# Kernel optimization log

Measured on AMD Instinct MI355X. Metric: run time of the kernel, lower is better.

Reference implementation:

```python
import jax, jax.numpy as jnp
import numpy as np

IN_DIM, HID, MEM, OUT = 512, 1024, 1024, 512
BATCH = 4096
HIST = 5  # hist_steps hard-coded in MMU.__init__

_LINEARS = [("inpgate", IN_DIM, HID), ("rec_inpgate", OUT, HID), ("mem_inpgate", MEM, HID),
            ("inp", IN_DIM, HID), ("rec_inp", OUT, HID),
            ("readgate", IN_DIM, MEM), ("rec_readgate", OUT, MEM), ("mem_readgate", MEM, MEM),
            ("decoder", HID, MEM),
            ("writegate", IN_DIM, MEM), ("rec_writegate", OUT, MEM), ("mem_writegate", MEM, MEM),
            ("encoder", MEM, HID)]


def setup_inputs() -> dict:
    key = jax.random.key(0)
    ks = iter(jax.random.split(key, 2 * len(_LINEARS) + 4))
    d = {"input": jax.random.normal(next(ks), (IN_DIM, BATCH), jnp.float32)}
    for name, fin, fout in _LINEARS:
        bound = 1.0 / np.sqrt(fin)  # torch nn.Linear default init range
        d["W_" + name] = jax.random.uniform(next(ks), (fout, fin), jnp.float32, -bound, bound)
        d["b_" + name] = jax.random.uniform(next(ks), (fout,), jnp.float32, -bound, bound)
    d["w_hid_out"] = jax.random.uniform(next(ks), (OUT, MEM), jnp.float32)  # torch.rand
    return d


def reference(input, W_inpgate, b_inpgate, W_rec_inpgate, b_rec_inpgate,
              W_mem_inpgate, b_mem_inpgate, W_inp, b_inp, W_rec_inp, b_rec_inp,
              W_readgate, b_readgate, W_rec_readgate, b_rec_readgate,
              W_mem_readgate, b_mem_readgate, W_decoder, b_decoder,
              W_writegate, b_writegate, W_rec_writegate, b_rec_writegate,
              W_mem_writegate, b_mem_writegate, W_encoder, b_encoder, w_hid_out):
    B = input.shape[1]
    lin = lambda x, W, b: x @ W.T + b
    # fresh module: history is zeros except last slot = current input (transposed to [B, in])
    xs = jnp.concatenate([jnp.zeros((HIST - 1, B, IN_DIM), input.dtype), input.T[None]], axis=0)

    def step(carry, x):
        out, mem = carry  # [B, OUT], [B, MEM]
        block_inp = jax.nn.sigmoid(lin(x, W_inp, b_inp) + lin(out, W_rec_inp, b_rec_inp))
        inp_gate = jax.nn.sigmoid(lin(x, W_inpgate, b_inpgate) + lin(mem, W_mem_inpgate, b_mem_inpgate)
                                  + lin(out, W_rec_inpgate, b_rec_inpgate))
        read_gate = jax.nn.sigmoid(lin(x, W_readgate, b_readgate) + lin(mem, W_mem_readgate, b_mem_readgate)
                                   + lin(out, W_rec_readgate, b_rec_readgate))
        decoded_mem = lin(read_gate * mem, W_decoder, b_decoder)
        hidden = decoded_mem + block_inp * inp_gate  # [B, HID] (HID == MEM)
        write_gate = jax.nn.sigmoid(lin(x, W_writegate, b_writegate) + lin(mem, W_mem_writegate, b_mem_writegate)
                                    + lin(out, W_rec_writegate, b_rec_writegate))
        encoded = jnp.tanh(lin(hidden, W_encoder, b_encoder))
        mem = (1.0 - write_gate) * mem + write_gate * encoded
        out = hidden @ w_hid_out.T  # w_hid_out.mm(hidden.T).T
        return (out, mem), None

    init = (jnp.zeros((B, OUT), input.dtype), jnp.zeros((B, MEM), input.dtype))
    (out, _mem), _ = jax.lax.scan(step, init, xs)
    return out
```

## Files before the change

### kernel.cpp

```cpp
#include <hip/hip_runtime.h>
#include <hip/hip_bf16.h>
#include <math.h>

typedef __hip_bfloat16 bf16;
typedef __attribute__((ext_vector_type(8))) short s16x8;
typedef __attribute__((ext_vector_type(4))) float f32x4;

__device__ __forceinline__ float fsig(float x) {
  return __builtin_amdgcn_rcpf(1.0f + __expf(-x));
}
__device__ __forceinline__ float ftanh(float x) { return 2.0f * fsig(2.0f * x) - 1.0f; }
__device__ __forceinline__ float dot4(float4 a, float4 b) {
  return a.x * b.x + a.y * b.y + a.z * b.z + a.w * b.w;
}

__global__ void setup(const float* __restrict__ W_inp, const float* __restrict__ W_ig,
                      const float* __restrict__ W_rg, const float* __restrict__ W_ho,
                      const float* __restrict__ W_dec, const float* __restrict__ input,
                      const float* __restrict__ b_inp, const float* __restrict__ b_rinp,
                      const float* __restrict__ b_ig, const float* __restrict__ b_mig,
                      const float* __restrict__ b_rig, const float* __restrict__ b_wg,
                      const float* __restrict__ b_mwg, const float* __restrict__ b_rwg,
                      const float* __restrict__ b_dec, bf16* __restrict__ Wcat,
                      bf16* __restrict__ WhoB, bf16* __restrict__ Wcat2, bf16* __restrict__ Wdt,
                      bf16* __restrict__ Xb, float* __restrict__ out_s, float* __restrict__ mem_s,
                      float* __restrict__ hidv, float* __restrict__ wgv,
                      float* __restrict__ vout) {
  __shared__ float t[32][33];
  const int id = blockIdx.x, tid = threadIdx.x;
  if (id < 8198) {
    const int i = id * 256 + tid;
    if (i < 524288) {
      Wcat[i] = __float2bfloat16(W_inp[i]);
    } else if (i < 1048576) {
      Wcat[i] = __float2bfloat16(W_ig[i - 524288]);
    } else if (i < 1572864) {
      Wcat[i] = __float2bfloat16(W_rg[i - 1048576]);
    } else if (i < 2097152) {
      const int k = i - 1572864;
      const bf16 vv = __float2bfloat16(W_ho[k]);
      WhoB[k] = vv;
      Wcat2[(size_t)(k >> 10) * 2048 + (k & 1023)] = vv;
    } else if (i < 2098688) {
      const int tt = i - 2097152;
      if (tt < 512) out_s[tt] = 0.0f;
      else mem_s[tt - 512] = 0.0f;
    }
  } else if (id < 10246) {
    const int b = id - 8198;
    const int i0 = (b >> 7) * 32, b0 = (b & 127) * 32;
    const int tx = tid & 31, ty = tid >> 5;
#pragma unroll
    for (int r = ty; r < 32; r += 8) t[r][tx] = input[(size_t)(i0 + r) * 4096 + b0 + tx];
    __syncthreads();
#pragma unroll
    for (int r = ty; r < 32; r += 8)
      Xb[(size_t)(b0 + r) * 512 + i0 + tx] = __float2bfloat16(t[tx][r]);
  } else if (id < 11270) {
    const int b = id - 10246;
    const int j0 = (b >> 5) * 32, k0 = (b & 31) * 32;
    const int tx = tid & 31, ty = tid >> 5;
#pragma unroll
    for (int r = ty; r < 32; r += 8) t[r][tx] = W_dec[(size_t)(j0 + r) * 1024 + k0 + tx];
    __syncthreads();
#pragma unroll
    for (int r = ty; r < 32; r += 8)
      Wdt[(size_t)(k0 + r) * 1024 + j0 + tx] = __float2bfloat16(t[tx][r]);
  } else if (id < 11274) {
    const int j = (id - 11270) * 256 + tid;
    const float bi = fsig(b_inp[j] + b_rinp[j]);
    const float ig = fsig(b_ig[j] + b_mig[j] + b_rig[j]);
    hidv[j] = b_dec[j] + bi * ig;
    wgv[j] = fsig(b_wg[j] + b_mwg[j] + b_rwg[j]);
  } else {
    const int o = id - 11274;
    const float4 a = *(const float4*)(W_ho + (size_t)o * 1024 + tid * 4);
    const float4 b = *(const float4*)(b_dec + tid * 4);
    float s = dot4(a, b);
#pragma unroll
    for (int off = 32; off > 0; off >>= 1) s += __shfl_down(s, off, 64);
    if ((tid & 63) == 0) t[0][tid >> 6] = s;
    __syncthreads();
    if (tid == 0) vout[o] = t[0][0] + t[0][1] + t[0][2] + t[0][3];
  }
}

__global__ void step_gates(const float* __restrict__ Wri, const float* __restrict__ Wmig,
                           const float* __restrict__ Wrig, const float* __restrict__ Wmrg,
                           const float* __restrict__ Wrrg, const float* __restrict__ Wmwg,
                           const float* __restrict__ Wrwg, const float* __restrict__ b_inp,
                           const float* __restrict__ b_rinp, const float* __restrict__ b_ig,
                           const float* __restrict__ b_mig, const float* __restrict__ b_rig,
                           const float* __restrict__ b_rg, const float* __restrict__ b_mrg,
                           const float* __restrict__ b_rrg, const float* __restrict__ b_wg,
                           const float* __restrict__ b_mwg, const float* __restrict__ b_rwg,
                           const float* __restrict__ out_s, const float* __restrict__ mem_s,
                           float* __restrict__ rgm, float* __restrict__ h0v,
                           float* __restrict__ wgv) {
  __shared__ float red[7][4];
  const int j = blockIdx.x, tid = threadIdx.x, lane = tid & 63, wave = tid >> 6;
  const float4 z = make_float4(0.f, 0.f, 0.f, 0.f);
  const float4 o4 = (tid < 128) ? *(const float4*)(out_s + tid * 4) : z;
  const float4 m4 = *(const float4*)(mem_s + tid * 4);
  float p[7];
  p[0] = dot4((tid < 128) ? *(const float4*)(Wri + (size_t)j * 512 + tid * 4) : z, o4);
  p[1] = dot4(*(const float4*)(Wmig + (size_t)j * 1024 + tid * 4), m4);
  p[2] = dot4((tid < 128) ? *(const float4*)(Wrig + (size_t)j * 512 + tid * 4) : z, o4);
  p[3] = dot4(*(const float4*)(Wmrg + (size_t)j * 1024 + tid * 4), m4);
  p[4] = dot4((tid < 128) ? *(const float4*)(Wrrg + (size_t)j * 512 + tid * 4) : z, o4);
  p[5] = dot4(*(const float4*)(Wmwg + (size_t)j * 1024 + tid * 4), m4);
  p[6] = dot4((tid < 128) ? *(const float4*)(Wrwg + (size_t)j * 512 + tid * 4) : z, o4);
#pragma unroll
  for (int d = 0; d < 7; ++d) {
    float s = p[d];
#pragma unroll
    for (int off = 32; off > 0; off >>= 1) s += __shfl_down(s, off, 64);
    if (lane == 0) red[d][wave] = s;
  }
  __syncthreads();
  if (tid == 0) {
    float D[7];
#pragma unroll
    for (int d = 0; d < 7; ++d) D[d] = red[d][0] + red[d][1] + red[d][2] + red[d][3];
    const float abi = b_inp[j] + b_rinp[j] + D[0];
    const float aig = b_ig[j] + b_mig[j] + b_rig[j] + D[1] + D[2];
    const float arg = b_rg[j] + b_mrg[j] + b_rrg[j] + D[3] + D[4];
    const float awg = b_wg[j] + b_mwg[j] + b_rwg[j] + D[5] + D[6];
    rgm[j] = fsig(arg) * mem_s[j];
    h0v[j] = fsig(abi) * fsig(aig);
    wgv[j] = fsig(awg);
  }
}

__global__ void step_decode(const float* __restrict__ Wdec, const float* __restrict__ b_dec,
                            const float* __restrict__ rgm, const float* __restrict__ h0v,
                            float* __restrict__ hidv) {
  __shared__ float red[4];
  const int j = blockIdx.x, tid = threadIdx.x;
  const float4 a = *(const float4*)(Wdec + (size_t)j * 1024 + tid * 4);
  const float4 b = *(const float4*)(rgm + tid * 4);
  float s = dot4(a, b);
#pragma unroll
  for (int off = 32; off > 0; off >>= 1) s += __shfl_down(s, off, 64);
  if ((tid & 63) == 0) red[tid >> 6] = s;
  __syncthreads();
  if (tid == 0) hidv[j] = b_dec[j] + red[0] + red[1] + red[2] + red[3] + h0v[j];
}

__global__ void step_update(const float* __restrict__ Wenc, const float* __restrict__ b_enc,
                            const float* __restrict__ Who, const float* __restrict__ hidv,
                            const float* __restrict__ wgv, float* __restrict__ mem_s,
                            float* __restrict__ out_s) {
  __shared__ float red[4];
  const int id = blockIdx.x, tid = threadIdx.x;
  const float* row = (id < 1024) ? (Wenc + (size_t)id * 1024) : (Who + (size_t)(id - 1024) * 1024);
  const float4 a = *(const float4*)(row + tid * 4);
  const float4 b = *(const float4*)(hidv + tid * 4);
  float s = dot4(a, b);
#pragma unroll
  for (int off = 32; off > 0; off >>= 1) s += __shfl_down(s, off, 64);
  if ((tid & 63) == 0) red[tid >> 6] = s;
  __syncthreads();
  if (tid == 0) {
    const float d = red[0] + red[1] + red[2] + red[3];
    if (id < 1024) {
      const float wg = wgv[id];
      mem_s[id] = (1.0f - wg) * mem_s[id] + wg * ftanh(b_enc[id] + d);
    } else {
      out_s[id - 1024] = d;
    }
  }
}

__global__ __launch_bounds__(256) void update0_p(
    const float* __restrict__ Wenc, const float* __restrict__ b_enc,
    const float* __restrict__ Who, const float* __restrict__ hidv,
    const float* __restrict__ wgv, float* __restrict__ mem_s, float* __restrict__ out_s,
    const bf16* __restrict__ WhoB, const bf16* __restrict__ Wdt, float* __restrict__ P) {
  __shared__ char smem[16384];
  const int tid = threadIdx.x;
  if (blockIdx.x < 1536) {
    float* red = (float*)smem;
    const int id = blockIdx.x;
    const float* row =
        (id < 1024) ? (Wenc + (size_t)id * 1024) : (Who + (size_t)(id - 1024) * 1024);
    const float4 a = *(const float4*)(row + tid * 4);
    const float4 b = *(const float4*)(hidv + tid * 4);
    float s = dot4(a, b);
#pragma unroll
    for (int off = 32; off > 0; off >>= 1) s += __shfl_down(s, off, 64);
    if ((tid & 63) == 0) red[tid >> 6] = s;
    __syncthreads();
    if (tid == 0) {
      const float d = red[0] + red[1] + red[2] + red[3];
      if (id < 1024) {
        const float wg = wgv[id];
        mem_s[id] = (1.0f - wg) * mem_s[id] + wg * ftanh(b_enc[id] + d);
      } else {
        out_s[id - 1024] = d;
      }
    }
    return;
  }
  const int bi = blockIdx.x - 1536;
  const int wave = tid >> 6, lane = tid & 63;
  const int wm = wave >> 1, wn = wave & 1;
  const int m0 = ((bi >> 4) & 7) * 64, n0 = (bi & 15) * 64;
  const int kt0 = (bi >> 7) * 512;
  f32x4 acc[2][2] = {};
  for (int kt = kt0; kt < kt0 + 512; kt += 64) {
    __syncthreads();
#pragma unroll
    for (int i = 0; i < 2; ++i) {
      const int ci = i * 256 + tid;
      const int row = ci >> 3, ck = (ci & 7) ^ (row & 7);
      const bf16* g = WhoB + (size_t)(m0 + row) * 1024 + kt + ck * 8;
      const unsigned lofs = (unsigned)__builtin_amdgcn_readfirstlane((i * 256 + wave * 64) * 16);
      __builtin_amdgcn_global_load_lds(
          (const __attribute__((address_space(1))) void*)g,
          (__attribute__((address_space(3))) void*)(smem + lofs), 16, 0, 0);
    }
#pragma unroll
    for (int i = 0; i < 2; ++i) {
      const int ci = i * 256 + tid;
      const int row = ci >> 3, ck = (ci & 7) ^ (row & 7);
      const bf16* g = Wdt + (size_t)(n0 + row) * 1024 + kt + ck * 8;
      const unsigned lofs =
          (unsigned)__builtin_amdgcn_readfirstlane(8192 + (i * 256 + wave * 64) * 16);
      __builtin_amdgcn_global_load_lds(
          (const __attribute__((address_space(1))) void*)g,
          (__attribute__((address_space(3))) void*)(smem + lofs), 16, 0, 0);
    }
    __syncthreads();
#pragma unroll
    for (int ks = 0; ks < 2; ++ks) {
      const int ckk = ks * 4 + (lane >> 4);
      s16x8 af[2];
#pragma unroll
      for (int i = 0; i < 2; ++i) {
        const int R = wm * 32 + i * 16 + (lane & 15);
        af[i] = *(const s16x8*)(smem + (R * 8 + (ckk ^ (R & 7))) * 16);
      }
#pragma unroll
      for (int j = 0; j < 2; ++j) {
        const int R = wn * 32 + j * 16 + (lane & 15);
        const s16x8 bfr = *(const s16x8*)(smem + 8192 + (R * 8 + (ckk ^ (R & 7))) * 16);
#pragma unroll
        for (int i = 0; i < 2; ++i)
          acc[i][j] = __builtin_amdgcn_mfma_f32_16x16x32_bf16(af[i], bfr, acc[i][j], 0, 0, 0);
      }
    }
  }
  const int mb = (lane >> 4) * 4, nb = lane & 15;
#pragma unroll
  for (int i = 0; i < 2; ++i) {
#pragma unroll
    for (int j = 0; j < 2; ++j) {
      const int col = n0 + wn * 32 + j * 16 + nb;
#pragma unroll
      for (int r = 0; r < 4; ++r) {
        const int rowg = m0 + wm * 32 + i * 16 + mb + r;
        atomicAdd(P + (size_t)rowg * 1024 + col, acc[i][j][r]);
      }
    }
  }
}

__global__ void final_consts(const float* __restrict__ Wri, const float* __restrict__ Wmig,
                             const float* __restrict__ Wrig, const float* __restrict__ Wmrg,
                             const float* __restrict__ Wrrg, const float* __restrict__ b_inp,
                             const float* __restrict__ b_rinp, const float* __restrict__ b_ig,
                             const float* __restrict__ b_mig, const float* __restrict__ b_rig,
                             const float* __restrict__ b_rg, const float* __restrict__ b_mrg,
                             const float* __restrict__ b_rrg, const float* __restrict__ out_s,
                             const float* __restrict__ mem_s, const float* __restrict__ P,
                             float* __restrict__ ccat, bf16* __restrict__ Wcat2) {
  __shared__ float red[5][4];
  const int id = blockIdx.x, tid = threadIdx.x, lane = tid & 63, wave = tid >> 6;
  if (id < 1024) {
    const float4 z = make_float4(0.f, 0.f, 0.f, 0.f);
    const float4 o4 = (tid < 128) ? *(const float4*)(out_s + tid * 4) : z;
    const float4 m4 = *(const float4*)(mem_s + tid * 4);
    float p[5];
    p[0] = dot4((tid < 128) ? *(const float4*)(Wri + (size_t)id * 512 + tid * 4) : z, o4);
    p[1] = dot4(*(const float4*)(Wmig + (size_t)id * 1024 + tid * 4), m4);
    p[2] = dot4((tid < 128) ? *(const float4*)(Wrig + (size_t)id * 512 + tid * 4) : z, o4);
    p[3] = dot4(*(const float4*)(Wmrg + (size_t)id * 1024 + tid * 4), m4);
    p[4] = dot4((tid < 128) ? *(const float4*)(Wrrg + (size_t)id * 512 + tid * 4) : z, o4);
#pragma unroll
    for (int d = 0; d < 5; ++d) {
      float s = p[d];
#pragma unroll
      for (int off = 32; off > 0; off >>= 1) s += __shfl_down(s, off, 64);
      if (lane == 0) red[d][wave] = s;
    }
    __syncthreads();
    if (tid == 0) {
      float D[5];
#pragma unroll
      for (int d = 0; d < 5; ++d) D[d] = red[d][0] + red[d][1] + red[d][2] + red[d][3];
      ccat[id] = b_inp[id] + b_rinp[id] + D[0];
      ccat[1024 + id] = b_ig[id] + b_mig[id] + b_rig[id] + D[1] + D[2];
      ccat[2048 + id] = b_rg[id] + b_mrg[id] + b_rrg[id] + D[3] + D[4];
    }
  } else {
    const int idx = (id - 1024) * 256 + tid;
    const int q = idx >> 10, k = idx & 1023;
    Wcat2[(size_t)q * 2048 + 1024 + k] = __float2bfloat16(P[idx] * mem_s[k]);
  }
}

__global__ __launch_bounds__(256, 4) void gemm_gates(const bf16* __restrict__ A,
                                                     const bf16* __restrict__ Wcat,
                                                     const float* __restrict__ ccat,
                                                     bf16* __restrict__ Hcat) {
  __shared__ char smem[32768];
  const int tid = threadIdx.x, wave = tid >> 6, lane = tid & 63;
  const int wm = wave >> 1, wn = wave & 1;
  const int m0 = blockIdx.y * 64, n0 = blockIdx.x * 64;
  f32x4 acc[3][2][2] = {};

  for (int kt = 0; kt < 512; kt += 64) {
    __syncthreads();
#pragma unroll
    for (int i = 0; i < 2; ++i) {
      const int ci = i * 256 + tid;
      const int row = ci >> 3, ck = (ci & 7) ^ (row & 7);
      const bf16* g = A + (size_t)(m0 + row) * 512 + kt + ck * 8;
      const unsigned lofs = (unsigned)__builtin_amdgcn_readfirstlane((i * 256 + wave * 64) * 16);
      __builtin_amdgcn_global_load_lds(
          (const __attribute__((address_space(1))) void*)g,
          (__attribute__((address_space(3))) void*)(smem + lofs), 16, 0, 0);
    }
#pragma unroll
    for (int gI = 0; gI < 3; ++gI) {
      const bf16* Bp = Wcat + gI * 524288;
#pragma unroll
      for (int i = 0; i < 2; ++i) {
        const int ci = i * 256 + tid;
        const int row = ci >> 3, ck = (ci & 7) ^ (row & 7);
        const bf16* g = Bp + (size_t)(n0 + row) * 512 + kt + ck * 8;
        const unsigned lofs = (unsigned)__builtin_amdgcn_readfirstlane(
            8192 + gI * 8192 + (i * 256 + wave * 64) * 16);
        __builtin_amdgcn_global_load_lds(
            (const __attribute__((address_space(1))) void*)g,
            (__attribute__((address_space(3))) void*)(smem + lofs), 16, 0, 0);
      }
    }
    __syncthreads();

#pragma unroll
    for (int ks = 0; ks < 2; ++ks) {
      const int ckk = ks * 4 + (lane >> 4);
      s16x8 af[2];
#pragma unroll
      for (int i = 0; i < 2; ++i) {
        const int R = wm * 32 + i * 16 + (lane & 15);
        af[i] = *(const s16x8*)(smem + (R * 8 + (ckk ^ (R & 7))) * 16);
      }
#pragma unroll
      for (int gI = 0; gI < 3; ++gI) {
#pragma unroll
        for (int j = 0; j < 2; ++j) {
          const int R = wn * 32 + j * 16 + (lane & 15);
          const s16x8 bfr =
              *(const s16x8*)(smem + 8192 + gI * 8192 + (R * 8 + (ckk ^ (R & 7))) * 16);
#pragma unroll
          for (int i = 0; i < 2; ++i)
            acc[gI][i][j] =
                __builtin_amdgcn_mfma_f32_16x16x32_bf16(af[i], bfr, acc[gI][i][j], 0, 0, 0);
        }
      }
    }
  }

  __syncthreads();
  bf16* sm = (bf16*)smem;
  bf16* sr = (bf16*)smem + 5120;
  const int mb = (lane >> 4) * 4, nb = lane & 15;
#pragma unroll
  for (int i = 0; i < 2; ++i) {
#pragma unroll
    for (int j = 0; j < 2; ++j) {
      const int colL = wn * 32 + j * 16 + nb;
      const int jg = n0 + colL;
      const float c0 = ccat[jg], c1 = ccat[1024 + jg], c2 = ccat[2048 + jg];
#pragma unroll
      for (int r = 0; r < 4; ++r) {
        const int rowL = wm * 32 + i * 16 + mb + r;
        const float h = fsig(acc[0][i][j][r] + c0) * fsig(acc[1][i][j][r] + c1);
        const float rg = fsig(acc[2][i][j][r] + c2);
        sm[rowL * 80 + colL] = __float2bfloat16(h);
        sr[rowL * 80 + colL] = __float2bfloat16(rg);
      }
    }
  }
  __syncthreads();
#pragma unroll
  for (int pp = 0; pp < 2; ++pp) {
    const int c = pp * 256 + tid;
    const int row = c >> 3, cc = c & 7;
    const s16x8 v0 = *(const s16x8*)(sm + row * 80 + cc * 8);
    const s16x8 v1 = *(const s16x8*)(sr + row * 80 + cc * 8);
    *(s16x8*)(Hcat + (size_t)(m0 + row) * 2048 + n0 + cc * 8) = v0;
    *(s16x8*)(Hcat + (size_t)(m0 + row) * 2048 + 1024 + n0 + cc * 8) = v1;
  }
}

__global__ __launch_bounds__(256, 4) void gemm_out(const bf16* __restrict__ A,
                                                   const bf16* __restrict__ Bp,
                                                   const float* __restrict__ vout,
                                                   float* __restrict__ outF) {
  __shared__ char smem[16384];
  const int tid = threadIdx.x, wave = tid >> 6, lane = tid & 63;
  const int wm = wave >> 1, wn = wave & 1;
  const int m0 = blockIdx.y * 64, n0 = blockIdx.x * 64;
  f32x4 acc[2][2] = {};

  for (int kt = 0; kt < 2048; kt += 64) {
    __syncthreads();
#pragma unroll
    for (int i = 0; i < 2; ++i) {
      const int ci = i * 256 + tid;
      const int row = ci >> 3, ck = (ci & 7) ^ (row & 7);
      const bf16* g = A + (size_t)(m0 + row) * 2048 + kt + ck * 8;
      const unsigned lofs = (unsigned)__builtin_amdgcn_readfirstlane((i * 256 + wave * 64) * 16);
      __builtin_amdgcn_global_load_lds(
          (const __attribute__((address_space(1))) void*)g,
          (__attribute__((address_space(3))) void*)(smem + lofs), 16, 0, 0);
    }
#pragma unroll
    for (int i = 0; i < 2; ++i) {
      const int ci = i * 256 + tid;
      const int row = ci >> 3, ck = (ci & 7) ^ (row & 7);
      const bf16* g = Bp + (size_t)(n0 + row) * 2048 + kt + ck * 8;
      const unsigned lofs =
          (unsigned)__builtin_amdgcn_readfirstlane(8192 + (i * 256 + wave * 64) * 16);
      __builtin_amdgcn_global_load_lds(
          (const __attribute__((address_space(1))) void*)g,
          (__attribute__((address_space(3))) void*)(smem + lofs), 16, 0, 0);
    }
    __syncthreads();

#pragma unroll
    for (int ks = 0; ks < 2; ++ks) {
      const int ckk = ks * 4 + (lane >> 4);
      s16x8 af[2];
#pragma unroll
      for (int i = 0; i < 2; ++i) {
        const int R = wm * 32 + i * 16 + (lane & 15);
        af[i] = *(const s16x8*)(smem + (R * 8 + (ckk ^ (R & 7))) * 16);
      }
#pragma unroll
      for (int j = 0; j < 2; ++j) {
        const int R = wn * 32 + j * 16 + (lane & 15);
        const s16x8 bfr = *(const s16x8*)(smem + 8192 + (R * 8 + (ckk ^ (R & 7))) * 16);
#pragma unroll
        for (int i = 0; i < 2; ++i)
          acc[i][j] = __builtin_amdgcn_mfma_f32_16x16x32_bf16(af[i], bfr, acc[i][j], 0, 0, 0);
      }
    }
  }

  const int mb = (lane >> 4) * 4, nb = lane & 15;
#pragma unroll
  for (int i = 0; i < 2; ++i) {
#pragma unroll
    for (int j = 0; j < 2; ++j) {
      const int col = n0 + wn * 32 + j * 16 + nb;
#pragma unroll
      for (int r = 0; r < 4; ++r) {
        const int rowg = m0 + wm * 32 + i * 16 + mb + r;
        outF[(size_t)rowg * 512 + col] = acc[i][j][r] + vout[col];
      }
    }
  }
}

extern "C" void kernel_launch(void* const* d_in, const int* in_sizes, int n_in, void* d_out,
                              int out_size, void* d_ws, size_t ws_size, hipStream_t stream) {
  const float* input  = (const float*)d_in[0];
  const float* W_ig   = (const float*)d_in[1];  const float* b_ig   = (const float*)d_in[2];
  const float* W_rig  = (const float*)d_in[3];  const float* b_rig  = (const float*)d_in[4];
  const float* W_mig  = (const float*)d_in[5];  const float* b_mig  = (const float*)d_in[6];
  const float* W_inp  = (const float*)d_in[7];  const float* b_inp  = (const float*)d_in[8];
  const float* W_rinp = (const float*)d_in[9];  const float* b_rinp = (const float*)d_in[10];
  const float* W_rg   = (const float*)d_in[11]; const float* b_rg   = (const float*)d_in[12];
  const float* W_rrg  = (const float*)d_in[13]; const float* b_rrg  = (const float*)d_in[14];
  const float* W_mrg  = (const float*)d_in[15]; const float* b_mrg  = (const float*)d_in[16];
  const float* W_dec  = (const float*)d_in[17]; const float* b_dec  = (const float*)d_in[18];
  const float* W_wg   = (const float*)d_in[19]; const float* b_wg   = (const float*)d_in[20];
  const float* W_rwg  = (const float*)d_in[21]; const float* b_rwg  = (const float*)d_in[22];
  const float* W_mwg  = (const float*)d_in[23]; const float* b_mwg  = (const float*)d_in[24];
  const float* W_enc  = (const float*)d_in[25]; const float* b_enc  = (const float*)d_in[26];
  const float* W_ho   = (const float*)d_in[27];
  (void)W_wg; (void)W_rwg; (void)W_mwg;

  char* ws = (char*)d_ws;
  float* out_s = (float*)(ws + 0);
  float* mem_s = (float*)(ws + 4096);
  float* rgm   = (float*)(ws + 8192);
  float* h0v   = (float*)(ws + 12288);
  float* wgv   = (float*)(ws + 16384);
  float* hidv  = (float*)(ws + 20480);
  float* ccat  = (float*)(ws + 24576);
  float* vout  = (float*)(ws + 40960);
  float* P     = (float*)(ws + 65536);
  bf16* Xb     = (bf16*)(ws + 2162688);
  bf16* Wcat   = (bf16*)(ws + 6356992);
  bf16* WhoB   = (bf16*)(ws + 9502720);
  bf16* Wcat2  = (bf16*)(ws + 10551296);
  bf16* Wdt    = (bf16*)(ws + 12648448);
  bf16* Hcat   = (bf16*)(ws + 14745600);

  setup<<<11786, 256, 0, stream>>>(W_inp, W_ig, W_rg, W_ho, W_dec, input, b_inp, b_rinp, b_ig,
                                   b_mig, b_rig, b_wg, b_mwg, b_rwg, b_dec, Wcat, WhoB, Wcat2,
                                   Wdt, Xb, out_s, mem_s, hidv, wgv, vout);

  update0_p<<<1792, 256, 0, stream>>>(W_enc, b_enc, W_ho, hidv, wgv, mem_s, out_s, WhoB, Wdt, P);

  for (int s = 0; s < 3; ++s) {
    step_gates<<<1024, 256, 0, stream>>>(W_rinp, W_mig, W_rig, W_mrg, W_rrg, W_mwg, W_rwg, b_inp,
                                         b_rinp, b_ig, b_mig, b_rig, b_rg, b_mrg, b_rrg, b_wg,
                                         b_mwg, b_rwg, out_s, mem_s, rgm, h0v, wgv);
    step_decode<<<1024, 256, 0, stream>>>(W_dec, b_dec, rgm, h0v, hidv);
    step_update<<<1536, 256, 0, stream>>>(W_enc, b_enc, W_ho, hidv, wgv, mem_s, out_s);
  }

  final_consts<<<3072, 256, 0, stream>>>(W_rinp, W_mig, W_rig, W_mrg, W_rrg, b_inp, b_rinp, b_ig,
                                         b_mig, b_rig, b_rg, b_mrg, b_rrg, out_s, mem_s, P, ccat,
                                         Wcat2);

  gemm_gates<<<dim3(16, 64), 256, 0, stream>>>(Xb, Wcat, ccat, Hcat);

  gemm_out<<<dim3(8, 64), 256, 0, stream>>>(Hcat, Wcat2, vout, (float*)d_out);
}
```

Measured before the change: 230.7 us.

## Fold decoder into encoder/output via precomputed products, fusing step kernels

Precomputes E = W_enc·W_dec and reuses P = W_ho·W_dec with bf16 MFMA in the setup GEMM, plus bias projections W_enc·b_dec and W_ho·b_dec. Each recurrent step can then compute encoder and output directly from rgm and h0v in one fused kernel, dropping the separate decode launch and its dependency. The trade-off is an extra 1024x1024x1024 GEMM up front, more fp32 workspace traffic in each step (reading E and P rows alongside W_enc and W_ho), and bf16 rounding in the folded matrices.

Result: no change. 229.8 us (-0.4%).

```diff
diff --git a/kernel.cpp b/kernel.cpp
--- a/kernel.cpp
+++ b/kernel.cpp
@@ -13,22 +13,29 @@
 __device__ __forceinline__ float dot4(float4 a, float4 b) {
   return a.x * b.x + a.y * b.y + a.z * b.z + a.w * b.w;
 }
+__device__ __forceinline__ float wred(float s) {
+#pragma unroll
+  for (int off = 32; off > 0; off >>= 1) s += __shfl_down(s, off, 64);
+  return s;
+}
 
 __global__ void setup(const float* __restrict__ W_inp, const float* __restrict__ W_ig,
                       const float* __restrict__ W_rg, const float* __restrict__ W_ho,
-                      const float* __restrict__ W_dec, const float* __restrict__ input,
+                      const float* __restrict__ W_dec, const float* __restrict__ W_enc,
+                      const float* __restrict__ input,
                       const float* __restrict__ b_inp, const float* __restrict__ b_rinp,
                       const float* __restrict__ b_ig, const float* __restrict__ b_mig,
                       const float* __restrict__ b_rig, const float* __restrict__ b_wg,
                       const float* __restrict__ b_mwg, const float* __restrict__ b_rwg,
                       const float* __restrict__ b_dec, bf16* __restrict__ Wcat,
                       bf16* __restrict__ WhoB, bf16* __restrict__ Wcat2, bf16* __restrict__ Wdt,
-                      bf16* __restrict__ Xb, float* __restrict__ out_s, float* __restrict__ mem_s,
+                      bf16* __restrict__ WencB, bf16* __restrict__ Xb,
+                      float* __restrict__ out_s, float* __restrict__ mem_s,
                       float* __restrict__ hidv, float* __restrict__ wgv,
-                      float* __restrict__ vout) {
+                      float* __restrict__ vout, float* __restrict__ Web) {
   __shared__ float t[32][33];
   const int id = blockIdx.x, tid = threadIdx.x;
-  if (id < 8198) {
+  if (id < 12294) {
     const int i = id * 256 + tid;
     if (i < 524288) {
       Wcat[i] = __float2bfloat16(W_inp[i]);
@@ -45,9 +52,12 @@
       const int tt = i - 2097152;
       if (tt < 512) out_s[tt] = 0.0f;
       else mem_s[tt - 512] = 0.0f;
-    }
-  } else if (id < 10246) {
-    const int b = id - 8198;
+    } else if (i < 3147264) {
+      const int k = i - 2098688;
+      WencB[k] = __float2bfloat16(W_enc[k]);
+    }
+  } else if (id < 14342) {
+    const int b = id - 12294;
     const int i0 = (b >> 7) * 32, b0 = (b & 127) * 32;
     const int tx = tid & 31, ty = tid >> 5;
 #pragma unroll
@@ -56,8 +66,8 @@
 #pragma unroll
     for (int r = ty; r < 32; r += 8)
       Xb[(size_t)(b0 + r) * 512 + i0 + tx] = __float2bfloat16(t[tx][r]);
-  } else if (id < 11270) {
-    const int b = id - 10246;
+  } else if (id < 15366) {
+    const int b = id - 14342;
     const int j0 = (b >> 5) * 32, k0 = (b & 31) * 32;
     const int tx = tid & 31, ty = tid >> 5;
 #pragma unroll
@@ -66,22 +76,25 @@
 #pragma unroll
     for (int r = ty; r < 32; r += 8)
       Wdt[(size_t)(k0 + r) * 1024 + j0 + tx] = __float2bfloat16(t[tx][r]);
-  } else if (id < 11274) {
-    const int j = (id - 11270) * 256 + tid;
+  } else if (id < 15370) {
+    const int j = (id - 15366) * 256 + tid;
     const float bi = fsig(b_inp[j] + b_rinp[j]);
     const float ig = fsig(b_ig[j] + b_mig[j] + b_rig[j]);
     hidv[j] = b_dec[j] + bi * ig;
     wgv[j] = fsig(b_wg[j] + b_mwg[j] + b_rwg[j]);
   } else {
-    const int o = id - 11274;
-    const float4 a = *(const float4*)(W_ho + (size_t)o * 1024 + tid * 4);
+    const int o = id - 15370;
+    const float* row = (o < 512) ? (W_ho + (size_t)o * 1024) : (W_enc + (size_t)(o - 512) * 1024);
+    const float4 a = *(const float4*)(row + tid * 4);
     const float4 b = *(const float4*)(b_dec + tid * 4);
-    float s = dot4(a, b);
-#pragma unroll
-    for (int off = 32; off > 0; off >>= 1) s += __shfl_down(s, off, 64);
+    float s = wred(dot4(a, b));
     if ((tid & 63) == 0) t[0][tid >> 6] = s;
     __syncthreads();
-    if (tid == 0) vout[o] = t[0][0] + t[0][1] + t[0][2] + t[0][3];
+    if (tid == 0) {
+      const float d = t[0][0] + t[0][1] + t[0][2] + t[0][3];
+      if (o < 512) vout[o] = d;
+      else Web[o - 512] = d;
+    }
   }
 }
 
@@ -112,9 +125,7 @@
   p[6] = dot4((tid < 128) ? *(const float4*)(Wrwg + (size_t)j * 512 + tid * 4) : z, o4);
 #pragma unroll
   for (int d = 0; d < 7; ++d) {
-    float s = p[d];
-#pragma unroll
-    for (int off = 32; off > 0; off >>= 1) s += __shfl_down(s, off, 64);
+    float s = wred(p[d]);
     if (lane == 0) red[d][wave] = s;
   }
   __syncthreads();
@@ -132,51 +143,40 @@
   }
 }
 
-__global__ void step_decode(const float* __restrict__ Wdec, const float* __restrict__ b_dec,
-                            const float* __restrict__ rgm, const float* __restrict__ h0v,
-                            float* __restrict__ hidv) {
-  __shared__ float red[4];
-  const int j = blockIdx.x, tid = threadIdx.x;
-  const float4 a = *(const float4*)(Wdec + (size_t)j * 1024 + tid * 4);
-  const float4 b = *(const float4*)(rgm + tid * 4);
-  float s = dot4(a, b);
-#pragma unroll
-  for (int off = 32; off > 0; off >>= 1) s += __shfl_down(s, off, 64);
-  if ((tid & 63) == 0) red[tid >> 6] = s;
-  __syncthreads();
-  if (tid == 0) hidv[j] = b_dec[j] + red[0] + red[1] + red[2] + red[3] + h0v[j];
-}
-
-__global__ void step_update(const float* __restrict__ Wenc, const float* __restrict__ b_enc,
-                            const float* __restrict__ Who, const float* __restrict__ hidv,
-                            const float* __restrict__ wgv, float* __restrict__ mem_s,
-                            float* __restrict__ out_s) {
+__global__ void step_fuse(const float* __restrict__ E, const float* __restrict__ Wenc,
+                          const float* __restrict__ P, const float* __restrict__ Who,
+                          const float* __restrict__ b_enc, const float* __restrict__ Web,
+                          const float* __restrict__ vout, const float* __restrict__ rgm,
+                          const float* __restrict__ h0v, const float* __restrict__ wgv,
+                          float* __restrict__ mem_s, float* __restrict__ out_s) {
   __shared__ float red[4];
   const int id = blockIdx.x, tid = threadIdx.x;
-  const float* row = (id < 1024) ? (Wenc + (size_t)id * 1024) : (Who + (size_t)(id - 1024) * 1024);
-  const float4 a = *(const float4*)(row + tid * 4);
-  const float4 b = *(const float4*)(hidv + tid * 4);
-  float s = dot4(a, b);
-#pragma unroll
-  for (int off = 32; off > 0; off >>= 1) s += __shfl_down(s, off, 64);
+  const float4 r4 = *(const float4*)(rgm + tid * 4);
+  const float4 h4 = *(const float4*)(h0v + tid * 4);
+  const float* Ar = (id < 1024) ? (E + (size_t)id * 1024) : (P + (size_t)(id - 1024) * 1024);
+  const float* Br = (id < 1024) ? (Wenc + (size_t)id * 1024) : (Who + (size_t)(id - 1024) * 1024);
+  const float s1 = dot4(*(const float4*)(Ar + tid * 4), r4);
+  const float s2 = dot4(*(const float4*)(Br + tid * 4), h4);
+  const float s = wred(s1 + s2);
   if ((tid & 63) == 0) red[tid >> 6] = s;
   __syncthreads();
   if (tid == 0) {
     const float d = red[0] + red[1] + red[2] + red[3];
     if (id < 1024) {
       const float wg = wgv[id];
-      mem_s[id] = (1.0f - wg) * mem_s[id] + wg * ftanh(b_enc[id] + d);
+      mem_s[id] = (1.0f - wg) * mem_s[id] + wg * ftanh(b_enc[id] + Web[id] + d);
     } else {
-      out_s[id - 1024] = d;
-    }
-  }
-}
-
-__global__ __launch_bounds__(256) void update0_p(
+      out_s[id - 1024] = vout[id - 1024] + d;
+    }
+  }
+}
+
+__global__ __launch_bounds__(256) void update0_pe(
     const float* __restrict__ Wenc, const float* __restrict__ b_enc,
     const float* __restrict__ Who, const float* __restrict__ hidv,
     const float* __restrict__ wgv, float* __restrict__ mem_s, float* __restrict__ out_s,
-    const bf16* __restrict__ WhoB, const bf16* __restrict__ Wdt, float* __restrict__ P) {
+    const bf16* __restrict__ WhoB, const bf16* __restrict__ WencB,
+    const bf16* __restrict__ Wdt, float* __restrict__ P, float* __restrict__ E) {
   __shared__ char smem[16384];
   const int tid = threadIdx.x;
   if (blockIdx.x < 1536) {
@@ -186,9 +186,7 @@
         (id < 1024) ? (Wenc + (size_t)id * 1024) : (Who + (size_t)(id - 1024) * 1024);
     const float4 a = *(const float4*)(row + tid * 4);
     const float4 b = *(const float4*)(hidv + tid * 4);
-    float s = dot4(a, b);
-#pragma unroll
-    for (int off = 32; off > 0; off >>= 1) s += __shfl_down(s, off, 64);
+    float s = wred(dot4(a, b));
     if ((tid & 63) == 0) red[tid >> 6] = s;
     __syncthreads();
     if (tid == 0) {
@@ -203,10 +201,19 @@
     return;
   }
   const int bi = blockIdx.x - 1536;
+  const bf16* Ag;
+  float* Cg;
+  int m0, n0, kt0;
+  if (bi < 256) {
+    Ag = WhoB; Cg = P;
+    m0 = ((bi >> 4) & 7) * 64; n0 = (bi & 15) * 64; kt0 = (bi >> 7) * 512;
+  } else {
+    const int b2 = bi - 256;
+    Ag = WencB; Cg = E;
+    m0 = ((b2 >> 4) & 15) * 64; n0 = (b2 & 15) * 64; kt0 = (b2 >> 8) * 512;
+  }
   const int wave = tid >> 6, lane = tid & 63;
   const int wm = wave >> 1, wn = wave & 1;
-  const int m0 = ((bi >> 4) & 7) * 64, n0 = (bi & 15) * 64;
-  const int kt0 = (bi >> 7) * 512;
   f32x4 acc[2][2] = {};
   for (int kt = kt0; kt < kt0 + 512; kt += 64) {
     __syncthreads();
@@ -214,7 +221,7 @@
     for (int i = 0; i < 2; ++i) {
       const int ci = i * 256 + tid;
       const int row = ci >> 3, ck = (ci & 7) ^ (row & 7);
-      const bf16* g = WhoB + (size_t)(m0 + row) * 1024 + kt + ck * 8;
+      const bf16* g = Ag + (size_t)(m0 + row) * 1024 + kt + ck * 8;
       const unsigned lofs = (unsigned)__builtin_amdgcn_readfirstlane((i * 256 + wave * 64) * 16);
       __builtin_amdgcn_global_load_lds(
           (const __attribute__((address_space(1))) void*)g,
@@ -260,7 +267,7 @@
 #pragma unroll
       for (int r = 0; r < 4; ++r) {
         const int rowg = m0 + wm * 32 + i * 16 + mb + r;
-        atomicAdd(P + (size_t)rowg * 1024 + col, acc[i][j][r]);
+        atomicAdd(Cg + (size_t)rowg * 1024 + col, acc[i][j][r]);
       }
     }
   }
@@ -289,9 +296,7 @@
     p[4] = dot4((tid < 128) ? *(const float4*)(Wrrg + (size_t)id * 512 + tid * 4) : z, o4);
 #pragma unroll
     for (int d = 0; d < 5; ++d) {
-      float s = p[d];
-#pragma unroll
-      for (int off = 32; off > 0; off >>= 1) s += __shfl_down(s, off, 64);
+      float s = wred(p[d]);
       if (lane == 0) red[d][wave] = s;
     }
     __syncthreads();
@@ -494,7 +499,7 @@
   const float* W_mwg  = (const float*)d_in[23]; const float* b_mwg  = (const float*)d_in[24];
   const float* W_enc  = (const float*)d_in[25]; const float* b_enc  = (const float*)d_in[26];
   const float* W_ho   = (const float*)d_in[27];
-  (void)W_wg; (void)W_rwg; (void)W_mwg;
+  (void)W_wg;
 
   char* ws = (char*)d_ws;
   float* out_s = (float*)(ws + 0);
@@ -505,6 +510,7 @@
   float* hidv  = (float*)(ws + 20480);
   float* ccat  = (float*)(ws + 24576);
   float* vout  = (float*)(ws + 40960);
+  float* Web   = (float*)(ws + 45056);
   float* P     = (float*)(ws + 65536);
   bf16* Xb     = (bf16*)(ws + 2162688);
   bf16* Wcat   = (bf16*)(ws + 6356992);
@@ -512,19 +518,22 @@
   bf16* Wcat2  = (bf16*)(ws + 10551296);
   bf16* Wdt    = (bf16*)(ws + 12648448);
   bf16* Hcat   = (bf16*)(ws + 14745600);
-
-  setup<<<11786, 256, 0, stream>>>(W_inp, W_ig, W_rg, W_ho, W_dec, input, b_inp, b_rinp, b_ig,
-                                   b_mig, b_rig, b_wg, b_mwg, b_rwg, b_dec, Wcat, WhoB, Wcat2,
-                                   Wdt, Xb, out_s, mem_s, hidv, wgv, vout);
-
-  update0_p<<<1792, 256, 0, stream>>>(W_enc, b_enc, W_ho, hidv, wgv, mem_s, out_s, WhoB, Wdt, P);
+  float* E     = (float*)(ws + 31522816);
+  bf16* WencB  = (bf16*)(ws + 35717120);
+
+  setup<<<16906, 256, 0, stream>>>(W_inp, W_ig, W_rg, W_ho, W_dec, W_enc, input, b_inp, b_rinp,
+                                   b_ig, b_mig, b_rig, b_wg, b_mwg, b_rwg, b_dec, Wcat, WhoB,
+                                   Wcat2, Wdt, WencB, Xb, out_s, mem_s, hidv, wgv, vout, Web);
+
+  update0_pe<<<2304, 256, 0, stream>>>(W_enc, b_enc, W_ho, hidv, wgv, mem_s, out_s, WhoB, WencB,
+                                       Wdt, P, E);
 
   for (int s = 0; s < 3; ++s) {
     step_gates<<<1024, 256, 0, stream>>>(W_rinp, W_mig, W_rig, W_mrg, W_rrg, W_mwg, W_rwg, b_inp,
                                          b_rinp, b_ig, b_mig, b_rig, b_rg, b_mrg, b_rrg, b_wg,
                                          b_mwg, b_rwg, out_s, mem_s, rgm, h0v, wgv);
-    step_decode<<<1024, 256, 0, stream>>>(W_dec, b_dec, rgm, h0v, hidv);
-    step_update<<<1536, 256, 0, stream>>>(W_enc, b_enc, W_ho, hidv, wgv, mem_s, out_s);
+    step_fuse<<<1536, 256, 0, stream>>>(E, W_enc, P, W_ho, b_enc, Web, vout, rgm, h0v, wgv,
+                                        mem_s, out_s);
   }
 
   final_consts<<<3072, 256, 0, stream>>>(W_rinp, W_mig, W_rig, W_mrg, W_rrg, b_inp, b_rinp, b_ig,
```
